# Optimization experiments

Hardware: AMD Instinct MI355X
Metric: run time of the kernel (lower is better)

Reference implementation:

```python
import jax, jax.numpy as jnp
import numpy as np

B, SEQ, DIM = 4, 2048, 2048
NH, HD = 16, 128            # head_dim = dim // n_head
HID = 5632                  # int(2*(4*dim)/3) rounded up to multiple_of=256
EPS = 1e-5
THETA = 500000.0


def setup_inputs() -> dict:
    key = jax.random.key(0)
    ks = jax.random.split(key, 9)
    s = 0.02  # init scale keeps activations/logits well-conditioned
    x = jax.random.normal(ks[0], (B, SEQ, DIM), jnp.float32)
    wq = jax.random.normal(ks[1], (DIM, DIM), jnp.float32) * s
    wk = jax.random.normal(ks[2], (DIM, DIM), jnp.float32) * s
    wv = jax.random.normal(ks[3], (DIM, DIM), jnp.float32) * s
    wo = jax.random.normal(ks[4], (DIM, DIM), jnp.float32) * s
    w1 = jax.random.normal(ks[5], (DIM, HID), jnp.float32) * s
    w2 = jax.random.normal(ks[6], (HID, DIM), jnp.float32) * s
    w3 = jax.random.normal(ks[7], (DIM, HID), jnp.float32) * s
    attn_norm_w = jnp.ones((DIM,), jnp.float32)
    ffn_norm_w = jnp.ones((DIM,), jnp.float32)
    # RoPE tables (real/imag of freqs_cis), [seq, head_dim//2]
    inv = 1.0 / (THETA ** (jnp.arange(0, HD, 2, dtype=jnp.float32) / HD))
    ang = jnp.arange(SEQ, dtype=jnp.float32)[:, None] * inv[None, :]
    return dict(x=x, wq=wq, wk=wk, wv=wv, wo=wo, w1=w1, w2=w2, w3=w3,
                attn_norm_w=attn_norm_w, ffn_norm_w=ffn_norm_w,
                freqs_cos=jnp.cos(ang), freqs_sin=jnp.sin(ang))


def rmsnorm(x, w, eps=EPS):
    return x * jax.lax.rsqrt(jnp.mean(x * x, axis=-1, keepdims=True) + eps) * w


def rope(x, cos, sin):
    # x: [b, s, h, d]; pairs (d0,d1),(d2,d3),... treated as complex, multiplied by e^{i*ang}
    a, b = x[..., 0::2], x[..., 1::2]
    c = cos[None, :, None, :]
    s = sin[None, :, None, :]
    return jnp.stack([a * c - b * s, a * s + b * c], axis=-1).reshape(x.shape)


def block(x, wq, wk, wv, wo, w1, w2, w3, attn_norm_w, ffn_norm_w, freqs_cos, freqs_sin):
    b, s, d = x.shape
    # --- attention sublayer ---
    hn = rmsnorm(x, attn_norm_w)
    q = (hn @ wq).reshape(b, s, NH, HD)
    k = (hn @ wk).reshape(b, s, NH, HD)
    v = (hn @ wv).reshape(b, s, NH, HD)
    q = rope(q, freqs_cos, freqs_sin)
    k = rope(k, freqs_cos, freqs_sin)
    scores = jnp.einsum('bqhd,bkhd->bhqk', q, k) / np.float32(np.sqrt(HD))
    mask = jnp.triu(jnp.full((s, s), -jnp.inf, dtype=scores.dtype), k=1)
    p = jax.nn.softmax(scores + mask, axis=-1)
    attn = jnp.einsum('bhqk,bkhd->bqhd', p, v).reshape(b, s, d) @ wo
    h = x + attn
    # --- SwiGLU FFN sublayer ---
    fn = rmsnorm(h, ffn_norm_w)
    ffn = (jax.nn.silu(fn @ w1) * (fn @ w3)) @ w2
    return h + ffn


def reference(x, wq, wk, wv, wo, w1, w2, w3, attn_norm_w, ffn_norm_w, freqs_cos, freqs_sin):
    return block(x, wq, wk, wv, wo, w1, w2, w3, attn_norm_w, ffn_norm_w, freqs_cos, freqs_sin)
```

## Files before the change

kernel.cpp:

```cpp
#include <hip/hip_runtime.h>
#include <stdint.h>

#define DIMV 2048
#define SEQV 2048
#define NHV 16
#define HDV 128
#define HIDV 5632
#define NROWS 8192
#define LDP 6144

typedef short bf16x8 __attribute__((ext_vector_type(8)));
typedef float f32x4 __attribute__((ext_vector_type(4)));
typedef unsigned short u16x8 __attribute__((ext_vector_type(8)));

#define GLD16(src, dst) __builtin_amdgcn_global_load_lds( \
    (const __attribute__((address_space(1))) unsigned int*)(src), \
    (__attribute__((address_space(3))) unsigned int*)(dst), 16, 0, 0)

__device__ __forceinline__ float bf2f(unsigned short u){
  union { unsigned u; float f; } x; x.u = ((unsigned)u) << 16; return x.f;
}
__device__ __forceinline__ unsigned short f2bf(float f){
  union { float f; unsigned u; } x; x.f = f;
  unsigned r = x.u + 0x7fffu + ((x.u >> 16) & 1u);
  return (unsigned short)(r >> 16);
}

__global__ void transpose_cast(const float* __restrict__ in, unsigned short* __restrict__ out,
                               int R, int C){
  __shared__ alignas(16) unsigned short tile[32][33];
  int c0 = blockIdx.x * 32, r0 = blockIdx.y * 32;
  int tx = threadIdx.x, ty = threadIdx.y;
#pragma unroll
  for (int i = 0; i < 32; i += 8)
    tile[ty + i][tx] = f2bf(in[(long)(r0 + ty + i) * C + (c0 + tx)]);
  __syncthreads();
#pragma unroll
  for (int i = 0; i < 32; i += 8)
    out[(long)(c0 + ty + i) * R + (r0 + tx)] = tile[tx][ty + i];
}

__global__ void transpose_v(const unsigned short* __restrict__ packed, unsigned short* __restrict__ vt){
  __shared__ alignas(16) unsigned short tile[32][33];
  int bh = blockIdx.z;
  int b = bh >> 4, h = bh & 15;
  int d0 = blockIdx.y * 32, s0 = blockIdx.x * 32;
  int tx = threadIdx.x, ty = threadIdx.y;
  const unsigned short* src = packed + (long)b * SEQV * LDP + 4096 + (long)h * HDV;
  unsigned short* dst = vt + (long)bh * HDV * SEQV;
#pragma unroll
  for (int i = 0; i < 32; i += 8)
    tile[ty + i][tx] = src[(long)(s0 + ty + i) * LDP + d0 + tx];
  __syncthreads();
#pragma unroll
  for (int i = 0; i < 32; i += 8)
    dst[(long)(d0 + ty + i) * SEQV + s0 + tx] = tile[tx][ty + i];
}

__global__ __launch_bounds__(256) void rmsnorm_k(const float* __restrict__ x,
                                                 const float* __restrict__ w,
                                                 unsigned short* __restrict__ out){
  int row = blockIdx.x, t = threadIdx.x;
  const float* xr = x + (long)row * DIMV;
  float4 v0 = ((const float4*)xr)[t * 2];
  float4 v1 = ((const float4*)xr)[t * 2 + 1];
  float ss = v0.x*v0.x + v0.y*v0.y + v0.z*v0.z + v0.w*v0.w
           + v1.x*v1.x + v1.y*v1.y + v1.z*v1.z + v1.w*v1.w;
#pragma unroll
  for (int off = 32; off; off >>= 1) ss += __shfl_down(ss, off);
  __shared__ float red[4];
  if ((t & 63) == 0) red[t >> 6] = ss;
  __syncthreads();
  float tot = red[0] + red[1] + red[2] + red[3];
  float sc = rsqrtf(tot * (1.0f / DIMV) + 1e-5f);
  const float* wr = w + t * 8;
  float vv[8] = {v0.x, v0.y, v0.z, v0.w, v1.x, v1.y, v1.z, v1.w};
  u16x8 o;
#pragma unroll
  for (int e = 0; e < 8; e++) o[e] = f2bf(vv[e] * sc * wr[e]);
  *(u16x8*)(out + (long)row * DIMV + t * 8) = o;
}

#define SCHEDB() __builtin_amdgcn_sched_barrier(0)
#define SBAR()   __builtin_amdgcn_s_barrier()

template <int MODE>
__global__ __launch_bounds__(512, 2) void gemm256(const unsigned short* __restrict__ A, int lda,
                                                  const unsigned short* __restrict__ Bt,
                                                  unsigned short* __restrict__ Cb,
                                                  float* __restrict__ Cf,
                                                  const float* __restrict__ resid,
                                                  int ldc, int M, int N, int K){
  __shared__ alignas(16) unsigned short As[2][256 * 64];
  __shared__ alignas(16) unsigned short Bs[2][256 * 64];
  int m0 = blockIdx.y * 256, n0 = blockIdx.x * 256;
  int tid = threadIdx.x, w = tid >> 6, l = tid & 63;
  int wm = w >> 2, wn = w & 3;
  int l15 = l & 15, l4 = l >> 4;
  int sr8 = l >> 3, sl = l & 7;
  int nt = K / 64;

  f32x4 acc[8][4];
#pragma unroll
  for (int i = 0; i < 8; i++)
#pragma unroll
    for (int j = 0; j < 4; j++) acc[i][j] = (f32x4){0.f, 0.f, 0.f, 0.f};

#define GSTAGE(Gp, ld_, r0_, slab) { \
    _Pragma("unroll") \
    for (int r = 0; r < 2; r++){ \
      int row = (r * 8 + w) * 8 + sr8; \
      int cs = sl ^ (row & 7); \
      GLD16((Gp) + (long)((r0_) + row) * (ld_) + cs * 8, (slab) + (r * 8 + w) * 512); \
    } }
#define STAGE_A(tt, half) { int _t = (tt); if (_t < nt) GSTAGE(A + _t * 64, lda, m0 + (half) * 128, &As[_t & 1][(half) * 8192]) }
#define STAGE_B(tt, half) { int _t = (tt); if (_t < nt) GSTAGE(Bt + _t * 64, K, n0 + (half) * 128, &Bs[_t & 1][(half) * 8192]) }
#define LDA8(bb, mi, ks) (*(const bf16x8*)(&As[bb][(wm * 128 + (mi) * 16 + l15) * 64 + (((ks) * 4 + l4) ^ (l15 & 7)) * 8]))
#define LDB8(bb, ni, ks) (*(const bf16x8*)(&Bs[bb][(wn * 64 + (ni) * 16 + l15) * 64 + (((ks) * 4 + l4) ^ (l15 & 7)) * 8]))
#define Q_MFMA(AF, BF, MOFF, NOFF) { \
    _Pragma("unroll") \
    for (int mi = 0; mi < 4; mi++) \
      _Pragma("unroll") \
      for (int ni = 0; ni < 2; ni++) \
        _Pragma("unroll") \
        for (int ks = 0; ks < 2; ks++) \
          acc[mi + (MOFF)][ni + (NOFF)] = __builtin_amdgcn_mfma_f32_16x16x32_bf16(AF[mi][ks], BF[ni][ks], acc[mi + (MOFF)][ni + (NOFF)], 0, 0, 0); }

  bf16x8 a03[4][2], a47[4][2], b01[2][2], b23[2][2];

  STAGE_A(0, 0); STAGE_A(0, 1); STAGE_B(0, 0); STAGE_B(0, 1);
  STAGE_A(1, 0); STAGE_B(1, 0); STAGE_B(1, 1);
  asm volatile("s_waitcnt vmcnt(6)" ::: "memory");
  SBAR();
  SCHEDB();
#pragma unroll
  for (int mi = 0; mi < 4; mi++){ a03[mi][0] = LDA8(0, mi, 0); a03[mi][1] = LDA8(0, mi, 1); }
#pragma unroll
  for (int ni = 0; ni < 2; ni++){ b01[ni][0] = LDB8(0, ni, 0); b01[ni][1] = LDB8(0, ni, 1); }
  SCHEDB();

  for (int t = 0; t < nt; t++){
    int bi = t & 1;
#pragma unroll
    for (int mi = 0; mi < 4; mi++){ a47[mi][0] = LDA8(bi, mi + 4, 0); a47[mi][1] = LDA8(bi, mi + 4, 1); }
    STAGE_A(t + 1, 1);
    SCHEDB(); SBAR(); SCHEDB();
    __builtin_amdgcn_s_setprio(1);
    Q_MFMA(a03, b01, 0, 0);
    __builtin_amdgcn_s_setprio(0);
    SCHEDB(); SBAR();
#pragma unroll
    for (int ni = 0; ni < 2; ni++){ b23[ni][0] = LDB8(bi, ni + 2, 0); b23[ni][1] = LDB8(bi, ni + 2, 1); }
    STAGE_A(t + 2, 0);
    SCHEDB(); SBAR(); SCHEDB();
    __builtin_amdgcn_s_setprio(1);
    Q_MFMA(a47, b01, 4, 0);
    __builtin_amdgcn_s_setprio(0);
    SCHEDB(); SBAR();
    STAGE_B(t + 2, 0);
    SCHEDB(); SBAR(); SCHEDB();
    __builtin_amdgcn_s_setprio(1);
    Q_MFMA(a03, b23, 0, 2);
    __builtin_amdgcn_s_setprio(0);
    SCHEDB(); SBAR();
    STAGE_B(t + 2, 1);
    SCHEDB();
    if (t + 2 < nt) asm volatile("s_waitcnt vmcnt(6)" ::: "memory");
    else            asm volatile("s_waitcnt vmcnt(0)" ::: "memory");
    SBAR();
    SCHEDB();
    if (t + 1 < nt){
      int bj = bi ^ 1;
#pragma unroll
      for (int mi = 0; mi < 4; mi++){ a03[mi][0] = LDA8(bj, mi, 0); a03[mi][1] = LDA8(bj, mi, 1); }
#pragma unroll
      for (int ni = 0; ni < 2; ni++){ b01[ni][0] = LDB8(bj, ni, 0); b01[ni][1] = LDB8(bj, ni, 1); }
    }
    SCHEDB();
    __builtin_amdgcn_s_setprio(1);
    Q_MFMA(a47, b23, 4, 2);
    __builtin_amdgcn_s_setprio(0);
    SCHEDB(); SBAR();
  }
#undef GSTAGE
#undef STAGE_A
#undef STAGE_B
#undef LDA8
#undef LDB8
#undef Q_MFMA

#pragma unroll
  for (int mi = 0; mi < 8; mi++)
#pragma unroll
    for (int ni = 0; ni < 4; ni++)
#pragma unroll
      for (int r = 0; r < 4; r++){
        int row = m0 + wm * 128 + mi * 16 + l4 * 4 + r;
        int col = n0 + wn * 64 + ni * 16 + l15;
        long idx = (long)row * ldc + col;
        float v = acc[mi][ni][r];
        if (MODE == 0) Cb[idx] = f2bf(v);
        else           Cf[idx] = v + resid[idx];
      }
}

__global__ __launch_bounds__(512, 2) void ffn13_256(const unsigned short* __restrict__ A,
                                                    const unsigned short* __restrict__ B1t,
                                                    const unsigned short* __restrict__ B3t,
                                                    unsigned short* __restrict__ G,
                                                    int M, int N, int K){
  __shared__ alignas(16) unsigned short As[2][256 * 64];
  __shared__ alignas(16) unsigned short B1s[2][128 * 64];
  __shared__ alignas(16) unsigned short B3s[2][128 * 64];
  int m0 = blockIdx.y * 256, n0 = blockIdx.x * 128;
  int tid = threadIdx.x, w = tid >> 6, l = tid & 63;
  int wm = w >> 2, wn = w & 3;
  int l15 = l & 15, l4 = l >> 4;
  int sr8 = l >> 3, sl = l & 7;
  int nt = K / 64;

  f32x4 acc1[8][2], acc3[8][2];
#pragma unroll
  for (int i = 0; i < 8; i++)
#pragma unroll
    for (int j = 0; j < 2; j++){ acc1[i][j] = (f32x4){0.f,0.f,0.f,0.f}; acc3[i][j] = (f32x4){0.f,0.f,0.f,0.f}; }

#define GSTAGE(Gp, ld_, r0_, slab) { \
    _Pragma("unroll") \
    for (int r = 0; r < 2; r++){ \
      int row = (r * 8 + w) * 8 + sr8; \
      int cs = sl ^ (row & 7); \
      GLD16((Gp) + (long)((r0_) + row) * (ld_) + cs * 8, (slab) + (r * 8 + w) * 512); \
    } }
#define STAGE_A(tt, half) { int _t = (tt); if (_t < nt) GSTAGE(A + _t * 64, K, m0 + (half) * 128, &As[_t & 1][(half) * 8192]) }
#define STAGE_B1(tt) { int _t = (tt); if (_t < nt) GSTAGE(B1t + _t * 64, K, n0, &B1s[_t & 1][0]) }
#define STAGE_B3(tt) { int _t = (tt); if (_t < nt) GSTAGE(B3t + _t * 64, K, n0, &B3s[_t & 1][0]) }
#define LDA8(bb, mi, ks) (*(const bf16x8*)(&As[bb][(wm * 128 + (mi) * 16 + l15) * 64 + (((ks) * 4 + l4) ^ (l15 & 7)) * 8]))
#define LDB18(bb, ni, ks) (*(const bf16x8*)(&B1s[bb][(wn * 32 + (ni) * 16 + l15) * 64 + (((ks) * 4 + l4) ^ (l15 & 7)) * 8]))
#define LDB38(bb, ni, ks) (*(const bf16x8*)(&B3s[bb][(wn * 32 + (ni) * 16 + l15) * 64 + (((ks) * 4 + l4) ^ (l15 & 7)) * 8]))
#define Q_MFMA(AF, BF, ACC, MOFF) { \
    _Pragma("unroll") \
    for (int mi = 0; mi < 4; mi++) \
      _Pragma("unroll") \
      for (int ni = 0; ni < 2; ni++) \
        _Pragma("unroll") \
        for (int ks = 0; ks < 2; ks++) \
          ACC[mi + (MOFF)][ni] = __builtin_amdgcn_mfma_f32_16x16x32_bf16(AF[mi][ks], BF[ni][ks], ACC[mi + (MOFF)][ni], 0, 0, 0); }

  bf16x8 a03[4][2], a47[4][2], b1f[2][2], b3f[2][2];

  STAGE_A(0, 0); STAGE_A(0, 1); STAGE_B1(0); STAGE_B3(0);
  STAGE_A(1, 0); STAGE_B1(1); STAGE_B3(1);
  asm volatile("s_waitcnt vmcnt(6)" ::: "memory");
  SBAR();
  SCHEDB();
#pragma unroll
  for (int mi = 0; mi < 4; mi++){ a03[mi][0] = LDA8(0, mi, 0); a03[mi][1] = LDA8(0, mi, 1); }
#pragma unroll
  for (int ni = 0; ni < 2; ni++){ b1f[ni][0] = LDB18(0, ni, 0); b1f[ni][1] = LDB18(0, ni, 1); }
  SCHEDB();

  for (int t = 0; t < nt; t++){
    int bi = t & 1;
#pragma unroll
    for (int mi = 0; mi < 4; mi++){ a47[mi][0] = LDA8(bi, mi + 4, 0); a47[mi][1] = LDA8(bi, mi + 4, 1); }
    STAGE_A(t + 1, 1);
    SCHEDB(); SBAR(); SCHEDB();
    __builtin_amdgcn_s_setprio(1);
    Q_MFMA(a03, b1f, acc1, 0);
    __builtin_amdgcn_s_setprio(0);
    SCHEDB(); SBAR();
#pragma unroll
    for (int ni = 0; ni < 2; ni++){ b3f[ni][0] = LDB38(bi, ni, 0); b3f[ni][1] = LDB38(bi, ni, 1); }
    STAGE_A(t + 2, 0);
    SCHEDB(); SBAR(); SCHEDB();
    __builtin_amdgcn_s_setprio(1);
    Q_MFMA(a47, b1f, acc1, 4);
    __builtin_amdgcn_s_setprio(0);
    SCHEDB(); SBAR();
    STAGE_B1(t + 2);
    SCHEDB(); SBAR(); SCHEDB();
    __builtin_amdgcn_s_setprio(1);
    Q_MFMA(a03, b3f, acc3, 0);
    __builtin_amdgcn_s_setprio(0);
    SCHEDB(); SBAR();
    STAGE_B3(t + 2);
    SCHEDB();
    if (t + 2 < nt) asm volatile("s_waitcnt vmcnt(6)" ::: "memory");
    else            asm volatile("s_waitcnt vmcnt(0)" ::: "memory");
    SBAR();
    SCHEDB();
    if (t + 1 < nt){
      int bj = bi ^ 1;
#pragma unroll
      for (int mi = 0; mi < 4; mi++){ a03[mi][0] = LDA8(bj, mi, 0); a03[mi][1] = LDA8(bj, mi, 1); }
#pragma unroll
      for (int ni = 0; ni < 2; ni++){ b1f[ni][0] = LDB18(bj, ni, 0); b1f[ni][1] = LDB18(bj, ni, 1); }
    }
    SCHEDB();
    __builtin_amdgcn_s_setprio(1);
    Q_MFMA(a47, b3f, acc3, 4);
    __builtin_amdgcn_s_setprio(0);
    SCHEDB(); SBAR();
  }
#undef GSTAGE
#undef STAGE_A
#undef STAGE_B1
#undef STAGE_B3
#undef LDA8
#undef LDB18
#undef LDB38
#undef Q_MFMA

#pragma unroll
  for (int mi = 0; mi < 8; mi++)
#pragma unroll
    for (int ni = 0; ni < 2; ni++)
#pragma unroll
      for (int r = 0; r < 4; r++){
        int row = m0 + wm * 128 + mi * 16 + l4 * 4 + r;
        int col = n0 + wn * 32 + ni * 16 + l15;
        float a = acc1[mi][ni][r];
        float si = a * (1.f / (1.f + __expf(-a)));
        G[(long)row * N + col] = f2bf(si * acc3[mi][ni][r]);
      }
}

__global__ __launch_bounds__(256) void rope_k(unsigned short* __restrict__ p,
                                              const float* __restrict__ cosT,
                                              const float* __restrict__ sinT,
                                              float qscale){
  long idx = (long)blockIdx.x * 256 + threadIdx.x;
  int i = (int)(idx & 63);
  long t = idx >> 6;
  int h = (int)(t & 15);
  long row = t >> 4;
  int s = (int)(row & (SEQV - 1));
  float c = cosT[s * 64 + i], sn = sinT[s * 64 + i];
  long base = row * LDP + h * HDV + 2 * i;
  unsigned pq = *(unsigned*)(p + base);
  float a = bf2f((unsigned short)(pq & 0xffff)), b = bf2f((unsigned short)(pq >> 16));
  float ra = (a * c - b * sn) * qscale, rb = (a * sn + b * c) * qscale;
  *(unsigned*)(p + base) = (unsigned)f2bf(ra) | ((unsigned)f2bf(rb) << 16);
  unsigned pk = *(unsigned*)(p + base + 2048);
  a = bf2f((unsigned short)(pk & 0xffff)); b = bf2f((unsigned short)(pk >> 16));
  ra = a * c - b * sn; rb = a * sn + b * c;
  *(unsigned*)(p + base + 2048) = (unsigned)f2bf(ra) | ((unsigned)f2bf(rb) << 16);
}

__global__ __launch_bounds__(256) void attn_k(unsigned short* __restrict__ p,
                                              const unsigned short* __restrict__ vt){
  __shared__ alignas(16) unsigned short Ks[2][64 * 128];
  __shared__ alignas(16) unsigned short Vs[2][128 * 64];
  __shared__ alignas(16) unsigned short Ps[4][16 * 64];
  int qt = (gridDim.x - 1) - blockIdx.x;
  int bh = blockIdx.y;
  int b = bh >> 4, h = bh & 15;
  int tid = threadIdx.x, w = tid >> 6, l = tid & 63;
  int l15 = l & 15, l4 = l >> 4;
  int qrow0 = qt * 64 + w * 16;
  long baseQ = (long)b * SEQV * LDP + (long)h * HDV;
  long baseV = (long)bh * HDV * SEQV;

  bf16x8 qf[4];
#pragma unroll
  for (int dc = 0; dc < 4; dc++)
    qf[dc] = *(const bf16x8*)(p + baseQ + (long)(qrow0 + l15) * LDP + dc * 32 + l4 * 8);

  f32x4 acc[8];
#pragma unroll
  for (int df = 0; df < 8; df++) acc[df] = (f32x4){0.f, 0.f, 0.f, 0.f};
  float mOld[4], lsum[4];
#pragma unroll
  for (int r = 0; r < 4; r++){ mOld[r] = -1e30f; lsum[r] = 0.f; }

#define ATTN_STAGE(buf, kt) {                                                       \
    int k0 = (kt) * 64;                                                             \
    _Pragma("unroll")                                                               \
    for (int i = 0; i < 4; i++){                                                    \
      int row = w * 16 + i * 4 + (l >> 4);                                          \
      int slot = (l & 15) ^ (row & 7);                                              \
      GLD16(p + baseQ + 2048 + (long)(k0 + row) * LDP + slot * 8,                   \
            Ks[buf] + (w * 16 + i * 4) * 128);                                      \
    }                                                                               \
    _Pragma("unroll")                                                               \
    for (int i = 0; i < 4; i++){                                                    \
      int row = w * 32 + i * 8 + (l >> 3);                                          \
      int slot = (l & 7) ^ (row & 7);                                               \
      GLD16(vt + baseV + (long)row * SEQV + k0 + slot * 8,                          \
            Vs[buf] + (w * 32 + i * 8) * 64);                                       \
    } }

  int ntile = qt + 1;
  ATTN_STAGE(0, 0);
  asm volatile("s_waitcnt vmcnt(0)" ::: "memory");
  __syncthreads();
  int cur = 0;
  for (int tki = 0; tki < ntile; tki++){
    int k0 = tki * 64;
    if (tki + 1 < ntile) ATTN_STAGE(cur ^ 1, tki + 1);

    float s[4][4];
    __builtin_amdgcn_s_setprio(1);
#pragma unroll
    for (int kf = 0; kf < 4; kf++){
      f32x4 sf = (f32x4){0.f, 0.f, 0.f, 0.f};
#pragma unroll
      for (int dc = 0; dc < 4; dc++){
        bf16x8 kb = *(const bf16x8*)(Ks[cur] + (kf * 16 + l15) * 128 + (((dc * 4 + l4) ^ (l15 & 7)) * 8));
        sf = __builtin_amdgcn_mfma_f32_16x16x32_bf16(qf[dc], kb, sf, 0, 0, 0);
      }
      int key = k0 + kf * 16 + l15;
#pragma unroll
      for (int r = 0; r < 4; r++){
        int rowi = qrow0 + l4 * 4 + r;
        s[kf][r] = (key <= rowi) ? sf[r] : -1e30f;
      }
    }
    __builtin_amdgcn_s_setprio(0);
    float scale[4];
#pragma unroll
    for (int r = 0; r < 4; r++){
      float vmax = fmaxf(fmaxf(s[0][r], s[1][r]), fmaxf(s[2][r], s[3][r]));
      for (int mm = 8; mm; mm >>= 1) vmax = fmaxf(vmax, __shfl_xor(vmax, mm));
      float mNew = fmaxf(mOld[r], vmax);
      scale[r] = __expf(mOld[r] - mNew);
      float ps = 0.f;
#pragma unroll
      for (int kf = 0; kf < 4; kf++){
        float pp = __expf(s[kf][r] - mNew);
        s[kf][r] = pp;
        ps += pp;
      }
      for (int mm = 8; mm; mm >>= 1) ps += __shfl_xor(ps, mm);
      lsum[r] = lsum[r] * scale[r] + ps;
      mOld[r] = mNew;
    }
#pragma unroll
    for (int df = 0; df < 8; df++)
#pragma unroll
      for (int r = 0; r < 4; r++) acc[df][r] *= scale[r];
#pragma unroll
    for (int kf = 0; kf < 4; kf++)
#pragma unroll
      for (int r = 0; r < 4; r++){
        int row = l4 * 4 + r;
        int sidx = row * 64 + (((((kf * 16 + l15) * 2)) ^ ((row & 7) << 4)) >> 1);
        Ps[w][sidx] = f2bf(s[kf][r]);
      }
    __builtin_amdgcn_s_setprio(1);
#pragma unroll
    for (int kc = 0; kc < 2; kc++){
      bf16x8 pa = *(const bf16x8*)(Ps[w] + l15 * 64 + (((kc * 64 + l4 * 16) ^ ((l15 & 7) << 4)) >> 1));
#pragma unroll
      for (int df = 0; df < 8; df++){
        bf16x8 vb = *(const bf16x8*)(Vs[cur] + (df * 16 + l15) * 64 + (((kc * 4 + l4) ^ (l15 & 7)) * 8));
        acc[df] = __builtin_amdgcn_mfma_f32_16x16x32_bf16(pa, vb, acc[df], 0, 0, 0);
      }
    }
    __builtin_amdgcn_s_setprio(0);
    asm volatile("s_waitcnt vmcnt(0)" ::: "memory");
    __syncthreads();
    cur ^= 1;
  }
#pragma unroll
  for (int df = 0; df < 8; df++)
#pragma unroll
    for (int r = 0; r < 4; r++){
      int rows = qrow0 + l4 * 4 + r;
      p[baseQ + (long)rows * LDP + df * 16 + l15] = f2bf(acc[df][r] / lsum[r]);
    }
#undef ATTN_STAGE
}

extern "C" void kernel_launch(void* const* d_in, const int* in_sizes, int n_in,
                              void* d_out, int out_size, void* d_ws, size_t ws_size,
                              hipStream_t stream){
  const float* x    = (const float*)d_in[0];
  const float* wq   = (const float*)d_in[1];
  const float* wk   = (const float*)d_in[2];
  const float* wv   = (const float*)d_in[3];
  const float* wo   = (const float*)d_in[4];
  const float* w1   = (const float*)d_in[5];
  const float* w2   = (const float*)d_in[6];
  const float* w3   = (const float*)d_in[7];
  const float* anw  = (const float*)d_in[8];
  const float* fnw  = (const float*)d_in[9];
  const float* fcos = (const float*)d_in[10];
  const float* fsin = (const float*)d_in[11];

  char* ws = (char*)d_ws;
  size_t off = 0;
  auto alloc = [&](size_t bytes) -> void* {
    void* p = ws + off;
    off += (bytes + 255) & ~(size_t)255;
    return p;
  };
  const size_t SQ = (size_t)DIMV * DIMV * 2;
  const size_t SW = (size_t)DIMV * HIDV * 2;
  const size_t SA = (size_t)NROWS * DIMV * 2;
  const size_t SP = (size_t)NROWS * LDP * 2;

  unsigned short* wqT = (unsigned short*)alloc(SQ);
  unsigned short* wkT = (unsigned short*)alloc(SQ);
  unsigned short* wvT = (unsigned short*)alloc(SQ);
  unsigned short* woT = (unsigned short*)alloc(SQ);
  unsigned short* w1T = (unsigned short*)alloc(SW);
  unsigned short* w3T = (unsigned short*)alloc(SW);
  unsigned short* w2T = (unsigned short*)alloc(SW);
  unsigned short* hn  = (unsigned short*)alloc(SA);
  unsigned short* pk  = (unsigned short*)alloc(SP);
  unsigned short* vtb = hn;
  unsigned short* g   = pk;
  float* hf = (float*)d_out;
  (void)ws_size; (void)in_sizes; (void)n_in; (void)out_size;
  (void)wkT; (void)wvT;

  dim3 tb(32, 8);
  transpose_cast<<<dim3(DIMV/32, DIMV/32), tb, 0, stream>>>(wq, wqT, DIMV, DIMV);
  transpose_cast<<<dim3(DIMV/32, DIMV/32), tb, 0, stream>>>(wk, wkT, DIMV, DIMV);
  transpose_cast<<<dim3(DIMV/32, DIMV/32), tb, 0, stream>>>(wv, wvT, DIMV, DIMV);
  transpose_cast<<<dim3(DIMV/32, DIMV/32), tb, 0, stream>>>(wo, woT, DIMV, DIMV);
  transpose_cast<<<dim3(HIDV/32, DIMV/32), tb, 0, stream>>>(w1, w1T, DIMV, HIDV);
  transpose_cast<<<dim3(HIDV/32, DIMV/32), tb, 0, stream>>>(w3, w3T, DIMV, HIDV);
  transpose_cast<<<dim3(DIMV/32, HIDV/32), tb, 0, stream>>>(w2, w2T, HIDV, DIMV);

  rmsnorm_k<<<NROWS, 256, 0, stream>>>(x, anw, hn);

  gemm256<0><<<dim3(LDP/256, NROWS/256), 512, 0, stream>>>(hn, DIMV, wqT, pk, nullptr, nullptr, LDP, NROWS, LDP, DIMV);

  rope_k<<<(NROWS * NHV * 64) / 256, 256, 0, stream>>>(pk, fcos, fsin, 0.08838834764831845f);

  transpose_v<<<dim3(SEQV/32, HDV/32, 4 * NHV), tb, 0, stream>>>(pk, vtb);

  attn_k<<<dim3(SEQV/64, 4 * NHV), 256, 0, stream>>>(pk, vtb);

  gemm256<1><<<dim3(DIMV/256, NROWS/256), 512, 0, stream>>>(pk, LDP, woT, nullptr, hf, x, DIMV, NROWS, DIMV, DIMV);

  rmsnorm_k<<<NROWS, 256, 0, stream>>>(hf, fnw, hn);

  ffn13_256<<<dim3(HIDV/128, NROWS/256), 512, 0, stream>>>(hn, w1T, w3T, g, NROWS, HIDV, DIMV);

  gemm256<1><<<dim3(DIMV/256, NROWS/256), 512, 0, stream>>>(g, HIDV, w2T, nullptr, hf, (const float*)hf, DIMV, NROWS, DIMV, HIDV);
}
```

Measured before the change: 1.503 ms.

## Restructure GEMM main loops and enlarge attention query tile to 128 rows

The GEMM and FFN13 inner loops drop the cross-iteration register prefetch of the next tile's A/B fragments. Each iteration now loads its fragments from LDS with explicit lgkmcnt waits and changes the order in which global-to-LDS stages are issued. Separately, the attention kernel moves to 512 threads with 128 query rows per block, so each K/V tile load is shared by 8 waves and fewer blocks are launched. The GEMM change exposes more LDS latency, and with 128-row query tiles the causal-diagonal work is less evenly balanced across blocks.

```diff
diff --git a/kernel.cpp b/kernel.cpp
--- a/kernel.cpp
+++ b/kernel.cpp
@@ -115,9 +115,9 @@
     } }
 #define STAGE_A(tt, half) { int _t = (tt); if (_t < nt) GSTAGE(A + _t * 64, lda, m0 + (half) * 128, &As[_t & 1][(half) * 8192]) }
 #define STAGE_B(tt, half) { int _t = (tt); if (_t < nt) GSTAGE(Bt + _t * 64, K, n0 + (half) * 128, &Bs[_t & 1][(half) * 8192]) }
-#define LDA8(bb, mi, ks) (*(const bf16x8*)(&As[bb][(wm * 128 + (mi) * 16 + l15) * 64 + (((ks) * 4 + l4) ^ (l15 & 7)) * 8]))
-#define LDB8(bb, ni, ks) (*(const bf16x8*)(&Bs[bb][(wn * 64 + (ni) * 16 + l15) * 64 + (((ks) * 4 + l4) ^ (l15 & 7)) * 8]))
-#define Q_MFMA(AF, BF, MOFF, NOFF) { \
+#define LDA8(mi, ks) (*(const bf16x8*)(&As[bi][(wm * 128 + (mi) * 16 + l15) * 64 + (((ks) * 4 + l4) ^ (l15 & 7)) * 8]))
+#define LDB8(ni, ks) (*(const bf16x8*)(&Bs[bi][(wn * 64 + (ni) * 16 + l15) * 64 + (((ks) * 4 + l4) ^ (l15 & 7)) * 8]))
+#define MFMA4x2(AF, BF, MOFF, NOFF) { \
     _Pragma("unroll") \
     for (int mi = 0; mi < 4; mi++) \
       _Pragma("unroll") \
@@ -126,68 +126,61 @@
         for (int ks = 0; ks < 2; ks++) \
           acc[mi + (MOFF)][ni + (NOFF)] = __builtin_amdgcn_mfma_f32_16x16x32_bf16(AF[mi][ks], BF[ni][ks], acc[mi + (MOFF)][ni + (NOFF)], 0, 0, 0); }
 
-  bf16x8 a03[4][2], a47[4][2], b01[2][2], b23[2][2];
-
   STAGE_A(0, 0); STAGE_A(0, 1); STAGE_B(0, 0); STAGE_B(0, 1);
-  STAGE_A(1, 0); STAGE_B(1, 0); STAGE_B(1, 1);
-  asm volatile("s_waitcnt vmcnt(6)" ::: "memory");
-  SBAR();
-  SCHEDB();
-#pragma unroll
-  for (int mi = 0; mi < 4; mi++){ a03[mi][0] = LDA8(0, mi, 0); a03[mi][1] = LDA8(0, mi, 1); }
-#pragma unroll
-  for (int ni = 0; ni < 2; ni++){ b01[ni][0] = LDB8(0, ni, 0); b01[ni][1] = LDB8(0, ni, 1); }
-  SCHEDB();
+  STAGE_A(1, 0); STAGE_A(1, 1);
+  asm volatile("s_waitcnt vmcnt(4)" ::: "memory");
+  __syncthreads();
 
   for (int t = 0; t < nt; t++){
     int bi = t & 1;
-#pragma unroll
-    for (int mi = 0; mi < 4; mi++){ a47[mi][0] = LDA8(bi, mi + 4, 0); a47[mi][1] = LDA8(bi, mi + 4, 1); }
-    STAGE_A(t + 1, 1);
-    SCHEDB(); SBAR(); SCHEDB();
-    __builtin_amdgcn_s_setprio(1);
-    Q_MFMA(a03, b01, 0, 0);
-    __builtin_amdgcn_s_setprio(0);
-    SCHEDB(); SBAR();
-#pragma unroll
-    for (int ni = 0; ni < 2; ni++){ b23[ni][0] = LDB8(bi, ni + 2, 0); b23[ni][1] = LDB8(bi, ni + 2, 1); }
+    bf16x8 a03[4][2], a47[4][2], b01[2][2], b23[2][2];
+#pragma unroll
+    for (int mi = 0; mi < 4; mi++){ a03[mi][0] = LDA8(mi, 0); a03[mi][1] = LDA8(mi, 1); }
+#pragma unroll
+    for (int ni = 0; ni < 2; ni++){ b01[ni][0] = LDB8(ni, 0); b01[ni][1] = LDB8(ni, 1); }
+    STAGE_B(t + 1, 0);
+    SBAR();
+    asm volatile("s_waitcnt lgkmcnt(0)" ::: "memory");
+    SCHEDB();
+    __builtin_amdgcn_s_setprio(1);
+    MFMA4x2(a03, b01, 0, 0);
+    __builtin_amdgcn_s_setprio(0);
+    SBAR();
+#pragma unroll
+    for (int mi = 0; mi < 4; mi++){ a47[mi][0] = LDA8(mi + 4, 0); a47[mi][1] = LDA8(mi + 4, 1); }
+    STAGE_B(t + 1, 1);
+    SBAR();
+    asm volatile("s_waitcnt lgkmcnt(0)" ::: "memory");
+    SCHEDB();
+    __builtin_amdgcn_s_setprio(1);
+    MFMA4x2(a47, b01, 4, 0);
+    __builtin_amdgcn_s_setprio(0);
+    SBAR();
+#pragma unroll
+    for (int ni = 0; ni < 2; ni++){ b23[ni][0] = LDB8(ni + 2, 0); b23[ni][1] = LDB8(ni + 2, 1); }
     STAGE_A(t + 2, 0);
-    SCHEDB(); SBAR(); SCHEDB();
-    __builtin_amdgcn_s_setprio(1);
-    Q_MFMA(a47, b01, 4, 0);
-    __builtin_amdgcn_s_setprio(0);
-    SCHEDB(); SBAR();
-    STAGE_B(t + 2, 0);
-    SCHEDB(); SBAR(); SCHEDB();
-    __builtin_amdgcn_s_setprio(1);
-    Q_MFMA(a03, b23, 0, 2);
-    __builtin_amdgcn_s_setprio(0);
-    SCHEDB(); SBAR();
-    STAGE_B(t + 2, 1);
+    SBAR();
+    asm volatile("s_waitcnt lgkmcnt(0)" ::: "memory");
     SCHEDB();
-    if (t + 2 < nt) asm volatile("s_waitcnt vmcnt(6)" ::: "memory");
+    __builtin_amdgcn_s_setprio(1);
+    MFMA4x2(a03, b23, 0, 2);
+    __builtin_amdgcn_s_setprio(0);
+    SBAR();
+    STAGE_A(t + 2, 1);
+    SBAR();
+    __builtin_amdgcn_s_setprio(1);
+    MFMA4x2(a47, b23, 4, 2);
+    __builtin_amdgcn_s_setprio(0);
+    if (t + 2 < nt) asm volatile("s_waitcnt vmcnt(4)" ::: "memory");
     else            asm volatile("s_waitcnt vmcnt(0)" ::: "memory");
     SBAR();
-    SCHEDB();
-    if (t + 1 < nt){
-      int bj = bi ^ 1;
-#pragma unroll
-      for (int mi = 0; mi < 4; mi++){ a03[mi][0] = LDA8(bj, mi, 0); a03[mi][1] = LDA8(bj, mi, 1); }
-#pragma unroll
-      for (int ni = 0; ni < 2; ni++){ b01[ni][0] = LDB8(bj, ni, 0); b01[ni][1] = LDB8(bj, ni, 1); }
-    }
-    SCHEDB();
-    __builtin_amdgcn_s_setprio(1);
-    Q_MFMA(a47, b23, 4, 2);
-    __builtin_amdgcn_s_setprio(0);
-    SCHEDB(); SBAR();
   }
 #undef GSTAGE
 #undef STAGE_A
 #undef STAGE_B
 #undef LDA8
 #undef LDB8
-#undef Q_MFMA
+#undef MFMA4x2
 
 #pragma unroll
   for (int mi = 0; mi < 8; mi++)
@@ -235,10 +228,10 @@
 #define STAGE_A(tt, half) { int _t = (tt); if (_t < nt) GSTAGE(A + _t * 64, K, m0 + (half) * 128, &As[_t & 1][(half) * 8192]) }
 #define STAGE_B1(tt) { int _t = (tt); if (_t < nt) GSTAGE(B1t + _t * 64, K, n0, &B1s[_t & 1][0]) }
 #define STAGE_B3(tt) { int _t = (tt); if (_t < nt) GSTAGE(B3t + _t * 64, K, n0, &B3s[_t & 1][0]) }
-#define LDA8(bb, mi, ks) (*(const bf16x8*)(&As[bb][(wm * 128 + (mi) * 16 + l15) * 64 + (((ks) * 4 + l4) ^ (l15 & 7)) * 8]))
-#define LDB18(bb, ni, ks) (*(const bf16x8*)(&B1s[bb][(wn * 32 + (ni) * 16 + l15) * 64 + (((ks) * 4 + l4) ^ (l15 & 7)) * 8]))
-#define LDB38(bb, ni, ks) (*(const bf16x8*)(&B3s[bb][(wn * 32 + (ni) * 16 + l15) * 64 + (((ks) * 4 + l4) ^ (l15 & 7)) * 8]))
-#define Q_MFMA(AF, BF, ACC, MOFF) { \
+#define LDA8(mi, ks) (*(const bf16x8*)(&As[bi][(wm * 128 + (mi) * 16 + l15) * 64 + (((ks) * 4 + l4) ^ (l15 & 7)) * 8]))
+#define LDB18(ni, ks) (*(const bf16x8*)(&B1s[bi][(wn * 32 + (ni) * 16 + l15) * 64 + (((ks) * 4 + l4) ^ (l15 & 7)) * 8]))
+#define LDB38(ni, ks) (*(const bf16x8*)(&B3s[bi][(wn * 32 + (ni) * 16 + l15) * 64 + (((ks) * 4 + l4) ^ (l15 & 7)) * 8]))
+#define MFMA4x2(AF, BF, ACC, MOFF) { \
     _Pragma("unroll") \
     for (int mi = 0; mi < 4; mi++) \
       _Pragma("unroll") \
@@ -247,61 +240,54 @@
         for (int ks = 0; ks < 2; ks++) \
           ACC[mi + (MOFF)][ni] = __builtin_amdgcn_mfma_f32_16x16x32_bf16(AF[mi][ks], BF[ni][ks], ACC[mi + (MOFF)][ni], 0, 0, 0); }
 
-  bf16x8 a03[4][2], a47[4][2], b1f[2][2], b3f[2][2];
-
   STAGE_A(0, 0); STAGE_A(0, 1); STAGE_B1(0); STAGE_B3(0);
-  STAGE_A(1, 0); STAGE_B1(1); STAGE_B3(1);
-  asm volatile("s_waitcnt vmcnt(6)" ::: "memory");
-  SBAR();
-  SCHEDB();
-#pragma unroll
-  for (int mi = 0; mi < 4; mi++){ a03[mi][0] = LDA8(0, mi, 0); a03[mi][1] = LDA8(0, mi, 1); }
-#pragma unroll
-  for (int ni = 0; ni < 2; ni++){ b1f[ni][0] = LDB18(0, ni, 0); b1f[ni][1] = LDB18(0, ni, 1); }
-  SCHEDB();
+  STAGE_A(1, 0); STAGE_A(1, 1);
+  asm volatile("s_waitcnt vmcnt(4)" ::: "memory");
+  __syncthreads();
 
   for (int t = 0; t < nt; t++){
     int bi = t & 1;
-#pragma unroll
-    for (int mi = 0; mi < 4; mi++){ a47[mi][0] = LDA8(bi, mi + 4, 0); a47[mi][1] = LDA8(bi, mi + 4, 1); }
-    STAGE_A(t + 1, 1);
-    SCHEDB(); SBAR(); SCHEDB();
-    __builtin_amdgcn_s_setprio(1);
-    Q_MFMA(a03, b1f, acc1, 0);
-    __builtin_amdgcn_s_setprio(0);
-    SCHEDB(); SBAR();
-#pragma unroll
-    for (int ni = 0; ni < 2; ni++){ b3f[ni][0] = LDB38(bi, ni, 0); b3f[ni][1] = LDB38(bi, ni, 1); }
+    bf16x8 a03[4][2], a47[4][2], b1f[2][2], b3f[2][2];
+#pragma unroll
+    for (int mi = 0; mi < 4; mi++){ a03[mi][0] = LDA8(mi, 0); a03[mi][1] = LDA8(mi, 1); }
+#pragma unroll
+    for (int ni = 0; ni < 2; ni++){ b1f[ni][0] = LDB18(ni, 0); b1f[ni][1] = LDB18(ni, 1); }
+    STAGE_B1(t + 1);
+    SBAR();
+    asm volatile("s_waitcnt lgkmcnt(0)" ::: "memory");
+    SCHEDB();
+    __builtin_amdgcn_s_setprio(1);
+    MFMA4x2(a03, b1f, acc1, 0);
+    __builtin_amdgcn_s_setprio(0);
+    SBAR();
+#pragma unroll
+    for (int mi = 0; mi < 4; mi++){ a47[mi][0] = LDA8(mi + 4, 0); a47[mi][1] = LDA8(mi + 4, 1); }
+    STAGE_B3(t + 1);
+    SBAR();
+    asm volatile("s_waitcnt lgkmcnt(0)" ::: "memory");
+    SCHEDB();
+    __builtin_amdgcn_s_setprio(1);
+    MFMA4x2(a47, b1f, acc1, 4);
+    __builtin_amdgcn_s_setprio(0);
+    SBAR();
+#pragma unroll
+    for (int ni = 0; ni < 2; ni++){ b3f[ni][0] = LDB38(ni, 0); b3f[ni][1] = LDB38(ni, 1); }
     STAGE_A(t + 2, 0);
-    SCHEDB(); SBAR(); SCHEDB();
-    __builtin_amdgcn_s_setprio(1);
-    Q_MFMA(a47, b1f, acc1, 4);
-    __builtin_amdgcn_s_setprio(0);
-    SCHEDB(); SBAR();
-    STAGE_B1(t + 2);
-    SCHEDB(); SBAR(); SCHEDB();
-    __builtin_amdgcn_s_setprio(1);
-    Q_MFMA(a03, b3f, acc3, 0);
-    __builtin_amdgcn_s_setprio(0);
-    SCHEDB(); SBAR();
-    STAGE_B3(t + 2);
+    SBAR();
+    asm volatile("s_waitcnt lgkmcnt(0)" ::: "memory");
     SCHEDB();
-    if (t + 2 < nt) asm volatile("s_waitcnt vmcnt(6)" ::: "memory");
+    __builtin_amdgcn_s_setprio(1);
+    MFMA4x2(a03, b3f, acc3, 0);
+    __builtin_amdgcn_s_setprio(0);
+    SBAR();
+    STAGE_A(t + 2, 1);
+    SBAR();
+    __builtin_amdgcn_s_setprio(1);
+    MFMA4x2(a47, b3f, acc3, 4);
+    __builtin_amdgcn_s_setprio(0);
+    if (t + 2 < nt) asm volatile("s_waitcnt vmcnt(4)" ::: "memory");
     else            asm volatile("s_waitcnt vmcnt(0)" ::: "memory");
     SBAR();
-    SCHEDB();
-    if (t + 1 < nt){
-      int bj = bi ^ 1;
-#pragma unroll
-      for (int mi = 0; mi < 4; mi++){ a03[mi][0] = LDA8(bj, mi, 0); a03[mi][1] = LDA8(bj, mi, 1); }
-#pragma unroll
-      for (int ni = 0; ni < 2; ni++){ b1f[ni][0] = LDB18(bj, ni, 0); b1f[ni][1] = LDB18(bj, ni, 1); }
-    }
-    SCHEDB();
-    __builtin_amdgcn_s_setprio(1);
-    Q_MFMA(a47, b3f, acc3, 4);
-    __builtin_amdgcn_s_setprio(0);
-    SCHEDB(); SBAR();
   }
 #undef GSTAGE
 #undef STAGE_A
@@ -310,7 +296,7 @@
 #undef LDA8
 #undef LDB18
 #undef LDB38
-#undef Q_MFMA
+#undef MFMA4x2
 
 #pragma unroll
   for (int mi = 0; mi < 8; mi++)
@@ -348,17 +334,17 @@
   *(unsigned*)(p + base + 2048) = (unsigned)f2bf(ra) | ((unsigned)f2bf(rb) << 16);
 }
 
-__global__ __launch_bounds__(256) void attn_k(unsigned short* __restrict__ p,
+__global__ __launch_bounds__(512) void attn_k(unsigned short* __restrict__ p,
                                               const unsigned short* __restrict__ vt){
   __shared__ alignas(16) unsigned short Ks[2][64 * 128];
   __shared__ alignas(16) unsigned short Vs[2][128 * 64];
-  __shared__ alignas(16) unsigned short Ps[4][16 * 64];
+  __shared__ alignas(16) unsigned short Ps[8][16 * 64];
   int qt = (gridDim.x - 1) - blockIdx.x;
   int bh = blockIdx.y;
   int b = bh >> 4, h = bh & 15;
   int tid = threadIdx.x, w = tid >> 6, l = tid & 63;
   int l15 = l & 15, l4 = l >> 4;
-  int qrow0 = qt * 64 + w * 16;
+  int qrow0 = qt * 128 + w * 16;
   long baseQ = (long)b * SEQV * LDP + (long)h * HDV;
   long baseV = (long)bh * HDV * SEQV;
 
@@ -377,21 +363,21 @@
 #define ATTN_STAGE(buf, kt) {                                                       \
     int k0 = (kt) * 64;                                                             \
     _Pragma("unroll")                                                               \
-    for (int i = 0; i < 4; i++){                                                    \
-      int row = w * 16 + i * 4 + (l >> 4);                                          \
+    for (int i = 0; i < 2; i++){                                                    \
+      int row = w * 8 + i * 4 + (l >> 4);                                           \
       int slot = (l & 15) ^ (row & 7);                                              \
       GLD16(p + baseQ + 2048 + (long)(k0 + row) * LDP + slot * 8,                   \
-            Ks[buf] + (w * 16 + i * 4) * 128);                                      \
+            Ks[buf] + (w * 8 + i * 4) * 128);                                       \
     }                                                                               \
     _Pragma("unroll")                                                               \
-    for (int i = 0; i < 4; i++){                                                    \
-      int row = w * 32 + i * 8 + (l >> 3);                                          \
+    for (int i = 0; i < 2; i++){                                                    \
+      int row = w * 16 + i * 8 + (l >> 3);                                          \
       int slot = (l & 7) ^ (row & 7);                                               \
       GLD16(vt + baseV + (long)row * SEQV + k0 + slot * 8,                          \
-            Vs[buf] + (w * 32 + i * 8) * 64);                                       \
+            Vs[buf] + (w * 16 + i * 8) * 64);                                       \
     } }
 
-  int ntile = qt + 1;
+  int ntile = 2 * (qt + 1);
   ATTN_STAGE(0, 0);
   asm volatile("s_waitcnt vmcnt(0)" ::: "memory");
   __syncthreads();
@@ -533,7 +519,7 @@
 
   transpose_v<<<dim3(SEQV/32, HDV/32, 4 * NHV), tb, 0, stream>>>(pk, vtb);
 
-  attn_k<<<dim3(SEQV/64, 4 * NHV), 256, 0, stream>>>(pk, vtb);
+  attn_k<<<dim3(SEQV/128, 4 * NHV), 512, 0, stream>>>(pk, vtb);
 
   gemm256<1><<<dim3(DIMV/256, NROWS/256), 512, 0, stream>>>(pk, LDP, woT, nullptr, hf, x, DIMV, NROWS, DIMV, DIMV);
 
```

After: 1.260 ms. -16.1%, faster.
